# Kernel optimization log

Measured on AMD Instinct MI355X. Metric: run time of the kernel, lower is better.

## Reference

```python
import jax, jax.numpy as jnp
import numpy as np

DILATED_KS = (7, 7)   # dilated_kernel_size (Hk, Wk)
SCALING = 1.0
GROUPS = 1
STRIDE = (1, 1)
PADDING = (3, 3)


def construct_kernel(weight, P):
    """Bilinear scatter-add of kernel_count weighted points into a dense
    (out, in//g, Hk, Wk) kernel. weight: (O, Cg, K), P: (2, Cg, K)."""
    Hk, Wk = DILATED_KS
    lim_h, lim_w = Hk // 2, Wk // 2
    O, Cg, K = weight.shape
    ph = jnp.clip(P[0] * SCALING, -lim_h, lim_h) + lim_h    # (Cg, K) in [0, Hk-1]
    pw = jnp.clip(P[1] * SCALING, -lim_w, lim_w) + lim_w    # (Cg, K) in [0, Wk-1]
    ih = jnp.floor(ph).astype(jnp.int32)
    iw = jnp.floor(pw).astype(jnp.int32)
    rh = ph - ih
    rw = pw - iw
    cidx = jnp.broadcast_to(jnp.arange(Cg)[:, None], (Cg, K))
    kern = jnp.zeros((O, Cg, Hk, Wk), dtype=weight.dtype)
    corners = [(0, 0, (1 - rh) * (1 - rw)),
               (0, 1, (1 - rh) * rw),
               (1, 0, rh * (1 - rw)),
               (1, 1, rh * rw)]
    for di, dj, frac in corners:
        # out-of-range corners (at the boundary) have zero frac; 'drop' discards them
        kern = kern.at[:, cidx, ih + di, iw + dj].add(weight * frac[None], mode='drop')
    return kern


def setup_inputs() -> dict:
    key = jax.random.key(0)
    k1, k2, k3, k4 = jax.random.split(key, 4)
    x = jax.random.normal(k1, (32, 128, 56, 56), dtype=jnp.float32)
    weight = jax.random.normal(k2, (128, 128, 9), dtype=jnp.float32) * 0.05
    P = jax.random.normal(k3, (2, 128, 9), dtype=jnp.float32)  # positions ~ N(0,1), clamped in fwd
    bias = jax.random.normal(k4, (128,), dtype=jnp.float32) * 0.05
    return {"x": x, "weight": weight, "P": P, "bias": bias}


def reference(x, weight, P, bias):
    kern = construct_kernel(weight, P)  # (O, Cg, 7, 7)
    out = jax.lax.conv_general_dilated(
        x, kern,
        window_strides=STRIDE,
        padding=[(PADDING[0], PADDING[0]), (PADDING[1], PADDING[1])],
        dimension_numbers=('NCHW', 'OIHW', 'NCHW'),
        feature_group_count=GROUPS)
    return out + bias[None, :, None, None]
```

## Files before the change

kernel.cpp:

```cpp
#include <hip/hip_runtime.h>
#include <stdint.h>

typedef short v8s  __attribute__((ext_vector_type(8)));
typedef float v16f __attribute__((ext_vector_type(16)));

#define KS    7
#define KPTS  9
#define OCH   128
#define CCH   128
#define NB    32
#define HW    56
#define PAD   3

#define HBLK  4
#define ROWS  10
#define WP    72
#define CCK   32
#define NCC   4
#define HP    62
#define ROWB  (WP*CCK*2)
#define XS_B  (ROWS*ROWB)
#define AB_B  (4*OCH*CCK*2)
#define SMEM_B (XS_B + AB_B)

__device__ __forceinline__ unsigned short f2bf(float f) {
  unsigned int u = __builtin_bit_cast(unsigned int, f);
  u += 0x7fffu + ((u >> 16) & 1u);
  return (unsigned short)(u >> 16);
}

__device__ __forceinline__ void gl_lds16(const void* g, void* l) {
  __builtin_amdgcn_global_load_lds(
      (const __attribute__((address_space(1))) unsigned int*)g,
      (__attribute__((address_space(3))) unsigned int*)l, 16, 0, 0);
}

__global__ __launch_bounds__(128) void build_kern(
    const float* __restrict__ wgt, const float* __restrict__ P,
    unsigned short* __restrict__ kb) {
  __shared__ float sm[OCH*49];
  const int c = blockIdx.x, o = threadIdx.x;
  float* mine = &sm[o*49];
  #pragma unroll
  for (int j = 0; j < 49; ++j) mine[j] = 0.f;
  for (int k = 0; k < KPTS; ++k) {
    const float ph = fminf(fmaxf(P[c*KPTS + k], -3.f), 3.f) + 3.f;
    const float pw = fminf(fmaxf(P[CCH*KPTS + c*KPTS + k], -3.f), 3.f) + 3.f;
    const int ih = (int)floorf(ph), iw = (int)floorf(pw);
    const float rh = ph - (float)ih, rw = pw - (float)iw;
    const float wt = wgt[(o*CCH + c)*KPTS + k];
    mine[ih*KS + iw] += wt*(1.f-rh)*(1.f-rw);
    if (iw+1 < KS) mine[ih*KS + iw+1] += wt*(1.f-rh)*rw;
    if (ih+1 < KS) mine[(ih+1)*KS + iw] += wt*rh*(1.f-rw);
    if (ih+1 < KS && iw+1 < KS) mine[(ih+1)*KS + iw+1] += wt*rh*rw;
  }
  const int cc = c >> 5, c32 = c & 31;
  const int kk = c32 >> 4, g = (c32 >> 3) & 1, j = c & 7;
  const int mt = o >> 5, l5 = o & 31;
  const size_t base = ((size_t)cc*49*8 + kk*4 + mt)*512 + (g*32 + l5)*8 + j;
  for (int tap = 0; tap < 49; ++tap)
    kb[base + (size_t)tap*4096] = f2bf(mine[tap]);
}

__global__ __launch_bounds__(256) void xpose(const float* __restrict__ x,
                                             unsigned short* __restrict__ xt) {
  __shared__ unsigned short lb[CCK][HW + 2];
  const int hp = blockIdx.x;
  const int cc = blockIdx.y;
  const int n  = blockIdx.z;
  const int t  = threadIdx.x;
  const int h  = hp - PAD;
  const bool valid = (unsigned)h < (unsigned)HW;
  if (valid) {
    const float* xb = x + ((size_t)(n*CCH + cc*CCK)*HW + h)*HW;
    #pragma unroll
    for (int k = 0; k < 7; ++k) {
      const int j = k*256 + t;
      const int c = j / HW, w = j % HW;
      lb[c][w] = f2bf(xb[(size_t)c*HW*HW + w]);
    }
  }
  __syncthreads();
  unsigned short* orow = xt + (size_t)((n*NCC + cc)*HP + hp)*(WP*4*8);
  for (int q = t; q < WP*4; q += 256) {
    const int kkg = q / WP, wq = q % WP;
    v8s v = (v8s){0,0,0,0,0,0,0,0};
    const int w = wq - PAD;
    if (valid && (unsigned)w < (unsigned)HW) {
      #pragma unroll
      for (int jj = 0; jj < 8; ++jj) v[jj] = (short)lb[kkg*8 + jj][w];
    }
    *(v8s*)&orow[q*8] = v;
  }
}

#define PF_A(T, FA)                                                           \
  {                                                                           \
    const unsigned short* ap = ab + (size_t)((T) & 3)*4096;                   \
    _Pragma("unroll")                                                         \
    for (int f = 0; f < 8; ++f)                                               \
      FA[f] = *(const v8s*)&ap[f*512 + lane*8];                               \
  }

#define PF_B(T, FB)                                                           \
  {                                                                           \
    const int kh = (T)/7, kw = (T) - kh*7;                                    \
    const int r = wv + kh;                                                    \
    _Pragma("unroll")                                                         \
    for (int kk = 0; kk < 2; ++kk)                                            \
      _Pragma("unroll")                                                       \
      for (int nt = 0; nt < 2; ++nt)                                          \
        FB[kk*2 + nt] = *(const v8s*)&xs[((size_t)((r*2 + kk)*2 + g)*WP +     \
                                          nt*32 + kw + l5)*8];                \
  }

#define MFMA_T(FA, FB)                                                        \
  {                                                                           \
    __builtin_amdgcn_s_setprio(1);                                            \
    _Pragma("unroll")                                                         \
    for (int kk = 0; kk < 2; ++kk)                                            \
      _Pragma("unroll")                                                       \
      for (int mt = 0; mt < 4; ++mt)                                          \
        _Pragma("unroll")                                                     \
        for (int nt = 0; nt < 2; ++nt)                                        \
          acc[mt][nt] = __builtin_amdgcn_mfma_f32_32x32x16_bf16(              \
              FA[kk*4 + mt], FB[kk*2 + nt], acc[mt][nt], 0, 0, 0);            \
    __builtin_amdgcn_s_setprio(0);                                            \
  }

__global__ __launch_bounds__(256, 2) void dcls_conv(
    const unsigned short* __restrict__ xt, const unsigned short* __restrict__ kb,
    const float* __restrict__ bias, float* __restrict__ out)
{
  extern __shared__ char smem[];
  unsigned short* xs = (unsigned short*)smem;
  unsigned short* ab = (unsigned short*)(smem + XS_B);

  const int n   = blockIdx.x;
  const int hb  = blockIdx.y;
  const int tid = threadIdx.x;
  const int lane = tid & 63;
  const int wv   = tid >> 6;
  const int l5   = lane & 31;
  const int g    = lane >> 5;

  v16f acc[4][2];
  {
    v16f z;
    #pragma unroll
    for (int i = 0; i < 16; ++i) z[i] = 0.f;
    #pragma unroll
    for (int m = 0; m < 4; ++m)
      #pragma unroll
      for (int t = 0; t < 2; ++t)
        acc[m][t] = z;
  }

  v8s fa0[8], fa1[8], fb0[4], fb1[4];

  for (int cc = 0; cc < NCC; ++cc) {
    const char* src = (const char*)xt + (size_t)((n*NCC + cc)*HP + hb*HBLK)*ROWB;
    for (int i = wv; i < 45; i += 4)
      gl_lds16(src + i*1024 + lane*16, (char*)xs + i*1024);
    const char* ks = (const char*)kb + (size_t)cc*49*8192;
    #pragma unroll
    for (int u = 0; u < 2; ++u)
      #pragma unroll
      for (int j = 0; j < 2; ++j)
        gl_lds16(ks + u*8192 + (wv*2 + j)*1024 + lane*16,
                 (char*)ab + u*8192 + (wv*2 + j)*1024);
    __syncthreads();

    PF_A(0, fa0)
    PF_B(0, fb0)

    #pragma unroll 1
    for (int p = 0; p < 24; ++p) {
      const int t0 = 2*p;
      {
        const int tp = t0 + 2;
        #pragma unroll
        for (int j = 0; j < 2; ++j)
          gl_lds16(ks + (size_t)tp*8192 + (wv*2 + j)*1024 + lane*16,
                   (char*)ab + (size_t)(tp & 3)*8192 + (wv*2 + j)*1024);
        const int tq = t0 + 3;
        if (tq < 49) {
          #pragma unroll
          for (int j = 0; j < 2; ++j)
            gl_lds16(ks + (size_t)tq*8192 + (wv*2 + j)*1024 + lane*16,
                     (char*)ab + (size_t)(tq & 3)*8192 + (wv*2 + j)*1024);
        }
      }
      PF_A(t0 + 1, fa1)
      PF_B(t0 + 1, fb1)
      MFMA_T(fa0, fb0)
      PF_B(t0 + 2, fb0)
      MFMA_T(fa1, fb1)
      __syncthreads();
      PF_A(t0 + 2, fa0)
    }
    MFMA_T(fa0, fb0)
    __syncthreads();
  }

  const int h = hb*HBLK + wv;
  #pragma unroll
  for (int mt = 0; mt < 4; ++mt) {
    #pragma unroll
    for (int rr = 0; rr < 16; ++rr) {
      const int o = mt*32 + (rr & 3) + 8*(rr >> 2) + 4*g;
      const float bs = bias[o];
      out[((size_t)(n*OCH + o)*HW + h)*HW + l5] = acc[mt][0][rr] + bs;
      if (l5 < 24)
        out[((size_t)(n*OCH + o)*HW + h)*HW + 32 + l5] = acc[mt][1][rr] + bs;
    }
  }
}

extern "C" void kernel_launch(void* const* d_in, const int* in_sizes, int n_in,
                              void* d_out, int out_size, void* d_ws, size_t ws_size,
                              hipStream_t stream) {
  const float* x    = (const float*)d_in[0];
  const float* wgt  = (const float*)d_in[1];
  const float* P    = (const float*)d_in[2];
  const float* bias = (const float*)d_in[3];
  float* out = (float*)d_out;

  unsigned short* kb = (unsigned short*)d_ws;
  unsigned short* xt = (unsigned short*)((char*)d_ws + (2u<<20));

  hipFuncSetAttribute((const void*)dcls_conv,
                      hipFuncAttributeMaxDynamicSharedMemorySize, SMEM_B);

  build_kern<<<CCH, OCH, 0, stream>>>(wgt, P, kb);
  xpose<<<dim3(HP, NCC, NB), 256, 0, stream>>>(x, xt);
  dcls_conv<<<dim3(NB, HW/HBLK), 256, SMEM_B, stream>>>(xt, kb, bias, out);
}
```

Baseline: 171.1 us.

## Compute two output rows per wave to reuse weight fragments across rows

Each wave now computes two output rows, so a block covers 8 rows instead of 4 and every A (weight) fragment loaded from LDS feeds twice as many MFMAs. The weight ring in LDS grows from 4 to 8 taps, filled four taps at a time with one barrier per four taps, replacing the old double-buffered register prefetch. Accumulators double to 2x4x2 v16f, and the launch bound drops to one block per CU, which means fewer resident waves for latency hiding. The grid shrinks to 32x7 blocks.

```diff
diff --git a/kernel.cpp b/kernel.cpp
--- a/kernel.cpp
+++ b/kernel.cpp
@@ -12,15 +12,15 @@
 #define HW    56
 #define PAD   3
 
-#define HBLK  4
-#define ROWS  10
+#define HBLK  8
+#define ROWS  14
 #define WP    72
 #define CCK   32
 #define NCC   4
 #define HP    62
 #define ROWB  (WP*CCK*2)
 #define XS_B  (ROWS*ROWB)
-#define AB_B  (4*OCH*CCK*2)
+#define AB_B  (8*4096*2)
 #define SMEM_B (XS_B + AB_B)
 
 __device__ __forceinline__ unsigned short f2bf(float f) {
@@ -94,41 +94,39 @@
   }
 }
 
-#define PF_A(T, FA)                                                           \
+#define TAP_COMPUTE(T)                                                        \
   {                                                                           \
-    const unsigned short* ap = ab + (size_t)((T) & 3)*4096;                   \
+    const int kh = (T)/7, kw = (T) - kh*7;                                    \
+    const unsigned short* ap = ab + (size_t)((T) & 7)*4096;                   \
+    v8s a[8], b[2][4];                                                        \
     _Pragma("unroll")                                                         \
     for (int f = 0; f < 8; ++f)                                               \
-      FA[f] = *(const v8s*)&ap[f*512 + lane*8];                               \
-  }
-
-#define PF_B(T, FB)                                                           \
-  {                                                                           \
-    const int kh = (T)/7, kw = (T) - kh*7;                                    \
-    const int r = wv + kh;                                                    \
+      a[f] = *(const v8s*)&ap[f*512 + lane*8];                                \
     _Pragma("unroll")                                                         \
-    for (int kk = 0; kk < 2; ++kk)                                            \
+    for (int d = 0; d < 2; ++d) {                                             \
+      const int r = wv*2 + d + kh;                                            \
       _Pragma("unroll")                                                       \
-      for (int nt = 0; nt < 2; ++nt)                                          \
-        FB[kk*2 + nt] = *(const v8s*)&xs[((size_t)((r*2 + kk)*2 + g)*WP +     \
-                                          nt*32 + kw + l5)*8];                \
-  }
-
-#define MFMA_T(FA, FB)                                                        \
-  {                                                                           \
+      for (int kk = 0; kk < 2; ++kk)                                          \
+        _Pragma("unroll")                                                     \
+        for (int nt = 0; nt < 2; ++nt)                                        \
+          b[d][kk*2 + nt] = *(const v8s*)&xs[((size_t)((r*2 + kk)*2 + g)*WP + \
+                                             nt*32 + kw + l5)*8];             \
+    }                                                                         \
     __builtin_amdgcn_s_setprio(1);                                            \
     _Pragma("unroll")                                                         \
-    for (int kk = 0; kk < 2; ++kk)                                            \
+    for (int d = 0; d < 2; ++d)                                               \
       _Pragma("unroll")                                                       \
-      for (int mt = 0; mt < 4; ++mt)                                          \
+      for (int kk = 0; kk < 2; ++kk)                                          \
         _Pragma("unroll")                                                     \
-        for (int nt = 0; nt < 2; ++nt)                                        \
-          acc[mt][nt] = __builtin_amdgcn_mfma_f32_32x32x16_bf16(              \
-              FA[kk*4 + mt], FB[kk*2 + nt], acc[mt][nt], 0, 0, 0);            \
+        for (int mt = 0; mt < 4; ++mt)                                        \
+          _Pragma("unroll")                                                   \
+          for (int nt = 0; nt < 2; ++nt)                                      \
+            acc[d][mt][nt] = __builtin_amdgcn_mfma_f32_32x32x16_bf16(         \
+                a[kk*4 + mt], b[d][kk*2 + nt], acc[d][mt][nt], 0, 0, 0);      \
     __builtin_amdgcn_s_setprio(0);                                            \
   }
 
-__global__ __launch_bounds__(256, 2) void dcls_conv(
+__global__ __launch_bounds__(256, 1) void dcls_conv(
     const unsigned short* __restrict__ xt, const unsigned short* __restrict__ kb,
     const float* __restrict__ bias, float* __restrict__ out)
 {
@@ -144,75 +142,71 @@
   const int l5   = lane & 31;
   const int g    = lane >> 5;
 
-  v16f acc[4][2];
+  v16f acc[2][4][2];
   {
     v16f z;
     #pragma unroll
     for (int i = 0; i < 16; ++i) z[i] = 0.f;
     #pragma unroll
-    for (int m = 0; m < 4; ++m)
-      #pragma unroll
-      for (int t = 0; t < 2; ++t)
-        acc[m][t] = z;
-  }
-
-  v8s fa0[8], fa1[8], fb0[4], fb1[4];
+    for (int d = 0; d < 2; ++d)
+      #pragma unroll
+      for (int m = 0; m < 4; ++m)
+        #pragma unroll
+        for (int t = 0; t < 2; ++t)
+          acc[d][m][t] = z;
+  }
 
   for (int cc = 0; cc < NCC; ++cc) {
     const char* src = (const char*)xt + (size_t)((n*NCC + cc)*HP + hb*HBLK)*ROWB;
-    for (int i = wv; i < 45; i += 4)
+    for (int i = wv; i < 63; i += 4)
       gl_lds16(src + i*1024 + lane*16, (char*)xs + i*1024);
     const char* ks = (const char*)kb + (size_t)cc*49*8192;
     #pragma unroll
-    for (int u = 0; u < 2; ++u)
+    for (int u = 0; u < 4; ++u)
       #pragma unroll
       for (int j = 0; j < 2; ++j)
-        gl_lds16(ks + u*8192 + (wv*2 + j)*1024 + lane*16,
-                 (char*)ab + u*8192 + (wv*2 + j)*1024);
-    __syncthreads();
-
-    PF_A(0, fa0)
-    PF_B(0, fb0)
+        gl_lds16(ks + (size_t)u*8192 + (wv*2 + j)*1024 + lane*16,
+                 (char*)ab + (size_t)u*8192 + (wv*2 + j)*1024);
+    asm volatile("s_waitcnt vmcnt(0)" ::: "memory");
+    __builtin_amdgcn_s_barrier();
 
     #pragma unroll 1
-    for (int p = 0; p < 24; ++p) {
-      const int t0 = 2*p;
-      {
-        const int tp = t0 + 2;
-        #pragma unroll
-        for (int j = 0; j < 2; ++j)
-          gl_lds16(ks + (size_t)tp*8192 + (wv*2 + j)*1024 + lane*16,
-                   (char*)ab + (size_t)(tp & 3)*8192 + (wv*2 + j)*1024);
-        const int tq = t0 + 3;
-        if (tq < 49) {
+    for (int p = 0; p < 12; ++p) {
+      const int tb = 4*p;
+      #pragma unroll
+      for (int j = 0; j < 4; ++j) {
+        const int T = tb + 4 + j;
+        if (T < 49) {
           #pragma unroll
-          for (int j = 0; j < 2; ++j)
-            gl_lds16(ks + (size_t)tq*8192 + (wv*2 + j)*1024 + lane*16,
-                     (char*)ab + (size_t)(tq & 3)*8192 + (wv*2 + j)*1024);
+          for (int q = 0; q < 2; ++q)
+            gl_lds16(ks + (size_t)T*8192 + (wv*2 + q)*1024 + lane*16,
+                     (char*)ab + (size_t)(T & 7)*8192 + (wv*2 + q)*1024);
         }
       }
-      PF_A(t0 + 1, fa1)
-      PF_B(t0 + 1, fb1)
-      MFMA_T(fa0, fb0)
-      PF_B(t0 + 2, fb0)
-      MFMA_T(fa1, fb1)
-      __syncthreads();
-      PF_A(t0 + 2, fa0)
-    }
-    MFMA_T(fa0, fb0)
+      TAP_COMPUTE(tb)
+      TAP_COMPUTE(tb + 1)
+      TAP_COMPUTE(tb + 2)
+      TAP_COMPUTE(tb + 3)
+      asm volatile("s_waitcnt vmcnt(0)" ::: "memory");
+      __builtin_amdgcn_s_barrier();
+    }
+    TAP_COMPUTE(48)
     __syncthreads();
   }
 
-  const int h = hb*HBLK + wv;
   #pragma unroll
-  for (int mt = 0; mt < 4; ++mt) {
-    #pragma unroll
-    for (int rr = 0; rr < 16; ++rr) {
-      const int o = mt*32 + (rr & 3) + 8*(rr >> 2) + 4*g;
-      const float bs = bias[o];
-      out[((size_t)(n*OCH + o)*HW + h)*HW + l5] = acc[mt][0][rr] + bs;
-      if (l5 < 24)
-        out[((size_t)(n*OCH + o)*HW + h)*HW + 32 + l5] = acc[mt][1][rr] + bs;
+  for (int d = 0; d < 2; ++d) {
+    const int h = hb*HBLK + wv*2 + d;
+    #pragma unroll
+    for (int mt = 0; mt < 4; ++mt) {
+      #pragma unroll
+      for (int rr = 0; rr < 16; ++rr) {
+        const int o = mt*32 + (rr & 3) + 8*(rr >> 2) + 4*g;
+        const float bs = bias[o];
+        out[((size_t)(n*OCH + o)*HW + h)*HW + l5] = acc[d][mt][0][rr] + bs;
+        if (l5 < 24)
+          out[((size_t)(n*OCH + o)*HW + h)*HW + 32 + l5] = acc[d][mt][1][rr] + bs;
+      }
     }
   }
 }
@@ -234,5 +228,5 @@
 
   build_kern<<<CCH, OCH, 0, stream>>>(wgt, P, kb);
   xpose<<<dim3(HP, NCC, NB), 256, 0, stream>>>(x, xt);
-  dcls_conv<<<dim3(NB, HW/HBLK), 256, SMEM_B, stream>>>(xt, kb, bias, out);
-}
+  dcls_conv<<<dim3(NB, KS), 256, SMEM_B, stream>>>(xt, kb, bias, out);
+}
```

Measured after the change: 175.7 us. 2.7% more time.

## Halve conv tile to 2 rows and 16-channel chunks with 128-thread blocks

Applied to the files above, without the earlier changes.

Shrinks the conv block to 2 output rows and 2 waves, and splits input channels into 8 chunks of 16 rather than 4 of 32. The packed kernel and transposed-input layouts and the MFMA fragment loads are reworked to match. The goal is more blocks and higher occupancy from a smaller LDS footprint. In exchange, each loaded weight tile is reused by only two waves, barriers per MFMA double, and halo rows are re-read more often.

```diff
diff --git a/kernel.cpp b/kernel.cpp
--- a/kernel.cpp
+++ b/kernel.cpp
@@ -12,15 +12,16 @@
 #define HW    56
 #define PAD   3
 
-#define HBLK  4
-#define ROWS  10
+#define HBLK  2
+#define ROWS  8
 #define WP    72
-#define CCK   32
-#define NCC   4
+#define CCK   16
+#define NCC   8
 #define HP    62
-#define ROWB  (WP*CCK*2)
+#define ROWB  (2*WP*8*2)
 #define XS_B  (ROWS*ROWB)
-#define AB_B  (4*OCH*CCK*2)
+#define SLOT_B 4096
+#define AB_B  (4*SLOT_B)
 #define SMEM_B (XS_B + AB_B)
 
 __device__ __forceinline__ unsigned short f2bf(float f) {
@@ -54,12 +55,12 @@
     if (ih+1 < KS) mine[(ih+1)*KS + iw] += wt*rh*(1.f-rw);
     if (ih+1 < KS && iw+1 < KS) mine[(ih+1)*KS + iw+1] += wt*rh*rw;
   }
-  const int cc = c >> 5, c32 = c & 31;
-  const int kk = c32 >> 4, g = (c32 >> 3) & 1, j = c & 7;
+  const int cc = c >> 4, cl = c & 15;
+  const int g = cl >> 3, j = c & 7;
   const int mt = o >> 5, l5 = o & 31;
-  const size_t base = ((size_t)cc*49*8 + kk*4 + mt)*512 + (g*32 + l5)*8 + j;
+  const size_t base = (((size_t)cc*49*4 + mt)*64 + g*32 + l5)*8 + j;
   for (int tap = 0; tap < 49; ++tap)
-    kb[base + (size_t)tap*4096] = f2bf(mine[tap]);
+    kb[base + (size_t)tap*2048] = f2bf(mine[tap]);
 }
 
 __global__ __launch_bounds__(256) void xpose(const float* __restrict__ x,
@@ -74,21 +75,23 @@
   if (valid) {
     const float* xb = x + ((size_t)(n*CCH + cc*CCK)*HW + h)*HW;
     #pragma unroll
-    for (int k = 0; k < 7; ++k) {
+    for (int k = 0; k < 4; ++k) {
       const int j = k*256 + t;
-      const int c = j / HW, w = j % HW;
-      lb[c][w] = f2bf(xb[(size_t)c*HW*HW + w]);
+      if (j < CCK*HW) {
+        const int c = j / HW, w = j % HW;
+        lb[c][w] = f2bf(xb[(size_t)c*HW*HW + w]);
+      }
     }
   }
   __syncthreads();
-  unsigned short* orow = xt + (size_t)((n*NCC + cc)*HP + hp)*(WP*4*8);
-  for (int q = t; q < WP*4; q += 256) {
-    const int kkg = q / WP, wq = q % WP;
+  unsigned short* orow = xt + (size_t)((n*NCC + cc)*HP + hp)*(2*WP*8);
+  for (int q = t; q < 2*WP; q += 256) {
+    const int g = q / WP, wq = q % WP;
     v8s v = (v8s){0,0,0,0,0,0,0,0};
     const int w = wq - PAD;
     if (valid && (unsigned)w < (unsigned)HW) {
       #pragma unroll
-      for (int jj = 0; jj < 8; ++jj) v[jj] = (short)lb[kkg*8 + jj][w];
+      for (int jj = 0; jj < 8; ++jj) v[jj] = (short)lb[g*8 + jj][w];
     }
     *(v8s*)&orow[q*8] = v;
   }
@@ -96,10 +99,10 @@
 
 #define PF_A(T, FA)                                                           \
   {                                                                           \
-    const unsigned short* ap = ab + (size_t)((T) & 3)*4096;                   \
+    const unsigned short* ap = ab + (size_t)((T) & 3)*2048;                   \
     _Pragma("unroll")                                                         \
-    for (int f = 0; f < 8; ++f)                                               \
-      FA[f] = *(const v8s*)&ap[f*512 + lane*8];                               \
+    for (int mt = 0; mt < 4; ++mt)                                            \
+      FA[mt] = *(const v8s*)&ap[mt*512 + lane*8];                             \
   }
 
 #define PF_B(T, FB)                                                           \
@@ -107,28 +110,23 @@
     const int kh = (T)/7, kw = (T) - kh*7;                                    \
     const int r = wv + kh;                                                    \
     _Pragma("unroll")                                                         \
-    for (int kk = 0; kk < 2; ++kk)                                            \
-      _Pragma("unroll")                                                       \
-      for (int nt = 0; nt < 2; ++nt)                                          \
-        FB[kk*2 + nt] = *(const v8s*)&xs[((size_t)((r*2 + kk)*2 + g)*WP +     \
-                                          nt*32 + kw + l5)*8];                \
+    for (int nt = 0; nt < 2; ++nt)                                            \
+      FB[nt] = *(const v8s*)&xs[((size_t)(r*2 + g)*WP + nt*32 + kw + l5)*8];  \
   }
 
 #define MFMA_T(FA, FB)                                                        \
   {                                                                           \
     __builtin_amdgcn_s_setprio(1);                                            \
     _Pragma("unroll")                                                         \
-    for (int kk = 0; kk < 2; ++kk)                                            \
+    for (int mt = 0; mt < 4; ++mt)                                            \
       _Pragma("unroll")                                                       \
-      for (int mt = 0; mt < 4; ++mt)                                          \
-        _Pragma("unroll")                                                     \
-        for (int nt = 0; nt < 2; ++nt)                                        \
-          acc[mt][nt] = __builtin_amdgcn_mfma_f32_32x32x16_bf16(              \
-              FA[kk*4 + mt], FB[kk*2 + nt], acc[mt][nt], 0, 0, 0);            \
+      for (int nt = 0; nt < 2; ++nt)                                          \
+        acc[mt][nt] = __builtin_amdgcn_mfma_f32_32x32x16_bf16(                \
+            FA[mt], FB[nt], acc[mt][nt], 0, 0, 0);                            \
     __builtin_amdgcn_s_setprio(0);                                            \
   }
 
-__global__ __launch_bounds__(256, 2) void dcls_conv(
+__global__ __launch_bounds__(128, 2) void dcls_conv(
     const unsigned short* __restrict__ xt, const unsigned short* __restrict__ kb,
     const float* __restrict__ bias, float* __restrict__ out)
 {
@@ -156,19 +154,20 @@
         acc[m][t] = z;
   }
 
-  v8s fa0[8], fa1[8], fb0[4], fb1[4];
+  v8s fa0[4], fa1[4], fb0[2], fb1[2];
 
   for (int cc = 0; cc < NCC; ++cc) {
     const char* src = (const char*)xt + (size_t)((n*NCC + cc)*HP + hb*HBLK)*ROWB;
-    for (int i = wv; i < 45; i += 4)
-      gl_lds16(src + i*1024 + lane*16, (char*)xs + i*1024);
-    const char* ks = (const char*)kb + (size_t)cc*49*8192;
+    #pragma unroll
+    for (int i = 0; i < 9; ++i)
+      gl_lds16(src + (wv + i*2)*1024 + lane*16, (char*)xs + (wv + i*2)*1024);
+    const char* ks = (const char*)kb + (size_t)cc*49*SLOT_B;
     #pragma unroll
     for (int u = 0; u < 2; ++u)
       #pragma unroll
       for (int j = 0; j < 2; ++j)
-        gl_lds16(ks + u*8192 + (wv*2 + j)*1024 + lane*16,
-                 (char*)ab + u*8192 + (wv*2 + j)*1024);
+        gl_lds16(ks + (size_t)u*SLOT_B + (wv*2 + j)*1024 + lane*16,
+                 (char*)ab + (size_t)u*SLOT_B + (wv*2 + j)*1024);
     __syncthreads();
 
     PF_A(0, fa0)
@@ -181,14 +180,14 @@
         const int tp = t0 + 2;
         #pragma unroll
         for (int j = 0; j < 2; ++j)
-          gl_lds16(ks + (size_t)tp*8192 + (wv*2 + j)*1024 + lane*16,
-                   (char*)ab + (size_t)(tp & 3)*8192 + (wv*2 + j)*1024);
+          gl_lds16(ks + (size_t)tp*SLOT_B + (wv*2 + j)*1024 + lane*16,
+                   (char*)ab + (size_t)(tp & 3)*SLOT_B + (wv*2 + j)*1024);
         const int tq = t0 + 3;
         if (tq < 49) {
           #pragma unroll
           for (int j = 0; j < 2; ++j)
-            gl_lds16(ks + (size_t)tq*8192 + (wv*2 + j)*1024 + lane*16,
-                     (char*)ab + (size_t)(tq & 3)*8192 + (wv*2 + j)*1024);
+            gl_lds16(ks + (size_t)tq*SLOT_B + (wv*2 + j)*1024 + lane*16,
+                     (char*)ab + (size_t)(tq & 3)*SLOT_B + (wv*2 + j)*1024);
         }
       }
       PF_A(t0 + 1, fa1)
@@ -234,5 +233,5 @@
 
   build_kern<<<CCH, OCH, 0, stream>>>(wgt, P, kb);
   xpose<<<dim3(HP, NCC, NB), 256, 0, stream>>>(x, xt);
-  dcls_conv<<<dim3(NB, HW/HBLK), 256, SMEM_B, stream>>>(xt, kb, bias, out);
-}
+  dcls_conv<<<dim3(NB, HW/HBLK), 128, SMEM_B, stream>>>(xt, kb, bias, out);
+}
```

After: 195.6 us. +14.3%, slower.
